# Kernel optimization log

Measured on AMD Instinct MI355X. Metric: run time of the kernel, lower is better.

Reference implementation:

```python
import jax, jax.numpy as jnp
import numpy as np

EPS = 1e-5

def _conv(x, w, b, stride, pad):
    y = jax.lax.conv_general_dilated(
        x, w, window_strides=(stride, stride),
        padding=[(pad, pad), (pad, pad)],
        dimension_numbers=('NCHW', 'OIHW', 'NCHW'))
    return y + b.reshape(1, -1, 1, 1)

def _bn(x, gamma, beta):
    # training-mode batch norm: per-channel batch statistics over (N, H, W)
    mean = jnp.mean(x, axis=(0, 2, 3), keepdims=True)
    var = jnp.var(x, axis=(0, 2, 3), keepdims=True)
    xn = (x - mean) * jax.lax.rsqrt(var + EPS)
    return gamma.reshape(1, -1, 1, 1) * xn + beta.reshape(1, -1, 1, 1)

def setup_inputs() -> dict:
    key = jax.random.key(0)
    ks = jax.random.split(key, 8)
    N, Cin, H, W = 64, 1024, 14, 14
    P = 256                      # planes (bottleneck width)
    Cout = P * 4                 # expansion = 4 -> 1024
    def kaiming(k, shape):
        fan_in = shape[1] * shape[2] * shape[3]
        return jax.random.normal(k, shape, jnp.float32) * np.float32(np.sqrt(2.0 / fan_in))
    return {
        'x':  jax.random.normal(ks[0], (N, Cin, H, W), jnp.float32),
        'w1': kaiming(ks[1], (P, Cin, 1, 1)),  'b1': jnp.zeros((P,), jnp.float32),
        'g1': jnp.ones((P,), jnp.float32),     'be1': jnp.zeros((P,), jnp.float32),
        'w2': kaiming(ks[2], (P, P, 3, 3)),    'b2': jnp.zeros((P,), jnp.float32),
        'g2': jnp.ones((P,), jnp.float32),     'be2': jnp.zeros((P,), jnp.float32),
        'w3': kaiming(ks[3], (Cout, P, 1, 1)), 'b3': jnp.zeros((Cout,), jnp.float32),
        'g3': jnp.ones((Cout,), jnp.float32),  'be3': jnp.zeros((Cout,), jnp.float32),
        'residual_scale': jnp.zeros((1,), jnp.float32),
    }

def reference(x, w1, b1, g1, be1, w2, b2, g2, be2, w3, b3, g3, be3, residual_scale):
    out = jax.nn.relu(_bn(_conv(x, w1, b1, 1, 0), g1, be1))   # 1x1 reduce
    out = jax.nn.relu(_bn(_conv(out, w2, b2, 1, 1), g2, be2)) # 3x3
    out = _bn(_conv(out, w3, b3, 1, 0), g3, be3)              # 1x1 expand
    out = jax.nn.softplus(residual_scale)[0] * out            # scaled residual branch
    out = x + out                                             # identity shortcut (stride=1, Cin==Cout)
    return jax.nn.relu(out)
```

## Files before the change

kernel.cpp:

```cpp
#include <hip/hip_runtime.h>
#include <hip/hip_bf16.h>
#include <cstdint>

#define NB   64
#define CIN  1024
#define HWSP 196
#define MTOT 12544
#define PL   256
#define COUT 1024

using f32x4 = __attribute__((ext_vector_type(4))) float;
using s16x8 = __attribute__((ext_vector_type(8))) short;

static __device__ __forceinline__ short f2bf(float f) {
  union { __hip_bfloat16 h; short s; } u;
  u.h = __float2bfloat16(f);
  return u.s;
}
static __device__ __forceinline__ float bf2f(short s) {
  union { float f; unsigned u; } x;
  x.u = ((unsigned)(unsigned short)s) << 16;
  return x.f;
}

static __device__ __forceinline__ void gload16(const void* g, void* l) {
  __builtin_amdgcn_global_load_lds((const __attribute__((address_space(1))) void*)g,
                                   (__attribute__((address_space(3))) void*)l, 16, 0, 0);
}

__global__ __launch_bounds__(256) void k_prep(const float* __restrict__ x,
                                              const float* __restrict__ w1,
                                              const float* __restrict__ w2,
                                              const float* __restrict__ w3,
                                              short* __restrict__ xb,
                                              short* __restrict__ w1b,
                                              short* __restrict__ w2b,
                                              short* __restrict__ w3b,
                                              float* __restrict__ statszero) {
  const int bid = blockIdx.x;
  if (bid < 2048) {
    __shared__ float tile[32][197];
    const int n = bid >> 5;
    const int c0 = (bid & 31) * 32;
    for (int idx = threadIdx.x; idx < 32 * 196; idx += 256) {
      int cl = idx / 196, hw = idx % 196;
      tile[cl][hw] = x[((size_t)(n * CIN + c0 + cl)) * HWSP + hw];
    }
    __syncthreads();
    for (int idx = threadIdx.x; idx < 196 * 32; idx += 256) {
      int hw = idx >> 5, cl = idx & 31;
      xb[((size_t)(n * HWSP + hw)) * CIN + c0 + cl] = f2bf(tile[cl][hw]);
    }
  } else if (bid < 6400) {
    int i = (bid - 2048) * 256 + threadIdx.x;
    if (i < 262144) w1b[i] = f2bf(w1[i]);
    int j = i - 262144;
    if (j >= 0 && j < 589824) {
      int co = j / 2304, rem = j % 2304;
      int d = rem >> 8, ci = rem & 255;
      w2b[j] = f2bf(w2[((size_t)(co * 256 + ci)) * 9 + d]);
    }
    int k = i - 851968;
    if (k >= 0 && k < 262144) w3b[k] = f2bf(w3[k]);
  } else {
    for (int k = threadIdx.x; k < 3136; k += 256) statszero[k] = 0.f;
  }
}

static __device__ __forceinline__ int swz(int row, int k16) {
  return row * 128 + (((unsigned)(k16 ^ (row & 7))) << 4);
}

template <int MODE, int K, int BM, int BN>
__global__ __launch_bounds__(256) void gemm_kernel(const short* __restrict__ A,
                                                   const short* __restrict__ Bw,
                                                   const float* __restrict__ bias,
                                                   short* __restrict__ Yb,
                                                   float* __restrict__ st,
                                                   int Nc,
                                                   const short* __restrict__ zerobuf) {
  constexpr int MI = BM / 32;
  constexpr int NJ = BN / 32;
  constexpr int ABYTES = BM * 128;
  __shared__ __align__(16) char lds[2][BM * 128 + BN * 128];

  const int m0 = blockIdx.x * BM;
  const int n0 = blockIdx.y * BN;
  const int t = threadIdx.x;
  const int lane = t & 63, wid = t >> 6;
  const int wm = wid >> 1, wn = wid & 1;
  const int g = lane >> 4, r = lane & 15;
  constexpr int NKT = K >> 6;

  const short* aSrc[MI];
  int aN[MI], aH[MI], aW[MI], aCi[MI];
#pragma unroll
  for (int q = 0; q < MI; ++q) {
    int chunk = t + q * 256;
    int row = chunk >> 3;
    int k16s = (chunk & 7) ^ (row & 7);
    if (MODE == 0) {
      aSrc[q] = A + (size_t)(m0 + row) * K + k16s * 8;
    } else {
      int m = m0 + row;
      int n_ = m / 196;
      int hw = m - n_ * 196;
      aN[q] = n_;
      aH[q] = hw / 14;
      aW[q] = hw - aH[q] * 14;
      aCi[q] = k16s * 8;
    }
  }
  const short* bSrc[NJ];
#pragma unroll
  for (int q = 0; q < NJ; ++q) {
    int chunk = t + q * 256;
    int row = chunk >> 3;
    int k16s = (chunk & 7) ^ (row & 7);
    bSrc[q] = Bw + (size_t)(n0 + row) * K + k16s * 8;
  }

  auto stage = [&](int buf, int kt) {
    const int k0 = kt << 6;
    char* dA = &lds[buf][0];
    char* dB = &lds[buf][ABYTES];
#pragma unroll
    for (int q = 0; q < MI; ++q) {
      const short* s;
      if (MODE == 0) {
        s = aSrc[q] + k0;
      } else {
        int d = kt >> 2;
        int dh = d / 3, dw = d - dh * 3;
        int hh = aH[q] + dh - 1, ww = aW[q] + dw - 1;
        s = ((unsigned)hh < 14u && (unsigned)ww < 14u)
                ? A + ((size_t)(aN[q] * 196 + hh * 14 + ww)) * 256 + (k0 & 255) + aCi[q]
                : zerobuf;
      }
      gload16(s, dA + (t + q * 256) * 16);
    }
#pragma unroll
    for (int q = 0; q < NJ; ++q)
      gload16(bSrc[q] + k0, dB + (t + q * 256) * 16);
  };

  f32x4 acc[MI][NJ] = {};
  auto compute = [&](int buf) {
    char* baseA = &lds[buf][0];
    char* baseB = &lds[buf][ABYTES];
#pragma unroll
    for (int ks = 0; ks < 2; ++ks) {
      s16x8 af[MI], bfr[NJ];
#pragma unroll
      for (int i = 0; i < MI; ++i)
        af[i] = *(const s16x8*)(baseA + swz(wm * (BM / 2) + i * 16 + r, ks * 4 + g));
#pragma unroll
      for (int j = 0; j < NJ; ++j)
        bfr[j] = *(const s16x8*)(baseB + swz(wn * (BN / 2) + j * 16 + r, ks * 4 + g));
#pragma unroll
      for (int i = 0; i < MI; ++i)
#pragma unroll
        for (int j = 0; j < NJ; ++j)
          acc[i][j] = __builtin_amdgcn_mfma_f32_16x16x32_bf16(af[i], bfr[j], acc[i][j], 0, 0, 0);
    }
  };

  stage(0, 0);
  __syncthreads();
  int cur = 0;
#pragma unroll 1
  for (int kt = 0; kt < NKT - 1; ++kt) {
    stage(cur ^ 1, kt + 1);
    compute(cur);
    __syncthreads();
    cur ^= 1;
  }
  compute(cur);

#pragma unroll
  for (int j = 0; j < NJ; ++j) {
    int col = n0 + wn * (BN / 2) + j * 16 + r;
    float bv = bias[col];
    float ps = 0.f, pq = 0.f;
#pragma unroll
    for (int i = 0; i < MI; ++i) {
      int row_base = m0 + wm * (BM / 2) + i * 16 + g * 4;
#pragma unroll
      for (int rr = 0; rr < 4; ++rr) {
        float v = acc[i][j][rr] + bv;
        ps += v;
        pq += v * v;
        Yb[(size_t)(row_base + rr) * Nc + col] = f2bf(v);
      }
    }
    ps += __shfl_xor(ps, 16);
    ps += __shfl_xor(ps, 32);
    pq += __shfl_xor(pq, 16);
    pq += __shfl_xor(pq, 32);
    if (lane < 16) {
      atomicAdd(&st[col], ps);
      atomicAdd(&st[Nc + col], pq);
    }
  }
}

__global__ __launch_bounds__(256) void k_apply(short* __restrict__ Yb,
                                               const float* __restrict__ st,
                                               const float* __restrict__ gamma,
                                               const float* __restrict__ beta) {
  __shared__ float lsc[256], lsh[256];
  const int t = threadIdx.x;
  {
    const float inv = 1.0f / 12544.0f;
    float mean = st[t] * inv;
    float var = st[256 + t] * inv - mean * mean;
    float s = gamma[t] * rsqrtf(var + 1e-5f);
    lsc[t] = s;
    lsh[t] = beta[t] - mean * s;
  }
  __syncthreads();
  size_t i8 = ((size_t)blockIdx.x * 256 + t) * 8;
  s16x8 v = *(const s16x8*)(Yb + i8);
  int c0 = (int)(i8 & 255);
#pragma unroll
  for (int e = 0; e < 8; ++e) {
    float f = bf2f(v[e]);
    v[e] = f2bf(fmaxf(lsc[c0 + e] * f + lsh[c0 + e], 0.f));
  }
  *(s16x8*)(Yb + i8) = v;
}

__global__ __launch_bounds__(256) void k_final(const float* __restrict__ x,
                                               const short* __restrict__ y3b,
                                               const float* __restrict__ st,
                                               const float* __restrict__ gamma,
                                               const float* __restrict__ beta,
                                               const float* __restrict__ rs,
                                               float* __restrict__ out) {
  __shared__ short ytile[64][198];
  __shared__ float lsc[64], lsh[64];
  const int n = blockIdx.x;
  const int co0 = blockIdx.y * 64;
  const int t = threadIdx.x;
  if (t < 64) {
    const float inv = 1.0f / 12544.0f;
    int c = co0 + t;
    float mean = st[c] * inv;
    float var = st[1024 + c] * inv - mean * mean;
    float s = gamma[c] * rsqrtf(var + 1e-5f);
    lsc[t] = s;
    lsh[t] = beta[c] - mean * s;
  }
#pragma unroll
  for (int iter = 0; iter < 49; ++iter) {
    int idx = iter * 256 + t;
    int hw = idx >> 6, c = idx & 63;
    ytile[c][hw] = y3b[((size_t)(n * 196 + hw)) * 1024 + co0 + c];
  }
  __syncthreads();
  float z = rs[0];
  float s = fmaxf(z, 0.f) + log1pf(expf(-fabsf(z)));
#pragma unroll
  for (int iter = 0; iter < 49; ++iter) {
    int idx = iter * 256 + t;
    int co = idx / 196, hw = idx - co * 196;
    size_t xi = ((size_t)(n * 1024 + co0 + co)) * 196 + hw;
    float v = bf2f(ytile[co][hw]);
    float o = x[xi] + s * (lsc[co] * v + lsh[co]);
    out[xi] = fmaxf(o, 0.f);
  }
}

extern "C" void kernel_launch(void* const* d_in, const int* in_sizes, int n_in,
                              void* d_out, int out_size, void* d_ws, size_t ws_size,
                              hipStream_t stream) {
  const float* x   = (const float*)d_in[0];
  const float* w1  = (const float*)d_in[1];
  const float* b1  = (const float*)d_in[2];
  const float* g1  = (const float*)d_in[3];
  const float* be1 = (const float*)d_in[4];
  const float* w2  = (const float*)d_in[5];
  const float* b2  = (const float*)d_in[6];
  const float* g2  = (const float*)d_in[7];
  const float* be2 = (const float*)d_in[8];
  const float* w3  = (const float*)d_in[9];
  const float* b3  = (const float*)d_in[10];
  const float* g3  = (const float*)d_in[11];
  const float* be3 = (const float*)d_in[12];
  const float* rs  = (const float*)d_in[13];
  float* out = (float*)d_out;
  char* ws = (char*)d_ws;

  size_t off = 0;
  auto alloc = [&](size_t bytes) {
    size_t o = off;
    off += (bytes + 255) & ~(size_t)255;
    return o;
  };
  short* xb  = (short*)(ws + alloc((size_t)MTOT * CIN * 2));
  short* w1b = (short*)(ws + alloc((size_t)262144 * 2));
  short* w2b = (short*)(ws + alloc((size_t)589824 * 2));
  short* w3b = (short*)(ws + alloc((size_t)262144 * 2));
  short* y1b = (short*)(ws + alloc((size_t)MTOT * PL * 2));
  short* y2b = (short*)(ws + alloc((size_t)MTOT * PL * 2));
  short* y3b = (short*)(ws + alloc((size_t)MTOT * COUT * 2));
  float* stats = (float*)(ws + alloc(12288 + 256));
  float* stat1 = stats, *stat2 = stats + 512, *stat3 = stats + 1024;
  short* zerobuf = (short*)(stats + 3072);

  k_prep<<<6401, 256, 0, stream>>>(x, w1, w2, w3, xb, w1b, w2b, w3b, stats);

  gemm_kernel<0, 1024, 128, 64><<<dim3(98, 4), 256, 0, stream>>>(xb, w1b, b1, y1b, stat1, 256, zerobuf);
  k_apply<<<1568, 256, 0, stream>>>(y1b, stat1, g1, be1);

  gemm_kernel<1, 2304, 64, 128><<<dim3(196, 2), 256, 0, stream>>>(y1b, w2b, b2, y2b, stat2, 256, zerobuf);
  k_apply<<<1568, 256, 0, stream>>>(y2b, stat2, g2, be2);

  gemm_kernel<0, 256, 128, 128><<<dim3(98, 8), 256, 0, stream>>>(y2b, w3b, b3, y3b, stat3, 1024, zerobuf);

  k_final<<<dim3(64, 16), 256, 0, stream>>>(x, y3b, stat3, g3, be3, rs, out);
}
```

Measured before the change: 129.5 us.

## Fuse batch-norm apply and ReLU into first two GEMMs via grid-wide barrier

Removes the two separate k_apply launches. Each GEMM block now accumulates bias-free channel statistics, waits on an atomic counter until all 392 blocks are done, then applies the normalization and ReLU straight from its accumulators before writing bf16 output. This saves a full read and write of the intermediate tensors and two launches. It relies on all 392 blocks being resident at once to avoid deadlock, and the spin wait adds a grid-wide stall at the end of each GEMM.

```diff
diff --git a/kernel.cpp b/kernel.cpp
--- a/kernel.cpp
+++ b/kernel.cpp
@@ -63,7 +63,7 @@
     int k = i - 851968;
     if (k >= 0 && k < 262144) w3b[k] = f2bf(w3[k]);
   } else {
-    for (int k = threadIdx.x; k < 3136; k += 256) statszero[k] = 0.f;
+    for (int k = threadIdx.x; k < 3200; k += 256) statszero[k] = 0.f;
   }
 }
 
@@ -71,13 +71,16 @@
   return row * 128 + (((unsigned)(k16 ^ (row & 7))) << 4);
 }
 
-template <int MODE, int K, int BM, int BN>
+template <int MODE, int K, int BM, int BN, int FUSE>
 __global__ __launch_bounds__(256) void gemm_kernel(const short* __restrict__ A,
                                                    const short* __restrict__ Bw,
                                                    const float* __restrict__ bias,
+                                                   const float* __restrict__ gamma,
+                                                   const float* __restrict__ beta,
                                                    short* __restrict__ Yb,
                                                    float* __restrict__ st,
-                                                   int Nc,
+                                                   unsigned* __restrict__ cnt,
+                                                   int nblk, int Nc,
                                                    const short* __restrict__ zerobuf) {
   constexpr int MI = BM / 32;
   constexpr int NJ = BN / 32;
@@ -177,57 +180,85 @@
   }
   compute(cur);
 
-#pragma unroll
-  for (int j = 0; j < NJ; ++j) {
-    int col = n0 + wn * (BN / 2) + j * 16 + r;
-    float bv = bias[col];
-    float ps = 0.f, pq = 0.f;
-#pragma unroll
-    for (int i = 0; i < MI; ++i) {
-      int row_base = m0 + wm * (BM / 2) + i * 16 + g * 4;
-#pragma unroll
-      for (int rr = 0; rr < 4; ++rr) {
-        float v = acc[i][j][rr] + bv;
-        ps += v;
-        pq += v * v;
-        Yb[(size_t)(row_base + rr) * Nc + col] = f2bf(v);
-      }
-    }
-    ps += __shfl_xor(ps, 16);
-    ps += __shfl_xor(ps, 32);
-    pq += __shfl_xor(pq, 16);
-    pq += __shfl_xor(pq, 32);
-    if (lane < 16) {
-      atomicAdd(&st[col], ps);
-      atomicAdd(&st[Nc + col], pq);
-    }
-  }
-}
-
-__global__ __launch_bounds__(256) void k_apply(short* __restrict__ Yb,
-                                               const float* __restrict__ st,
-                                               const float* __restrict__ gamma,
-                                               const float* __restrict__ beta) {
-  __shared__ float lsc[256], lsh[256];
-  const int t = threadIdx.x;
-  {
+  if (FUSE == 0) {
+#pragma unroll
+    for (int j = 0; j < NJ; ++j) {
+      int col = n0 + wn * (BN / 2) + j * 16 + r;
+      float bv = bias[col];
+      float ps = 0.f, pq = 0.f;
+#pragma unroll
+      for (int i = 0; i < MI; ++i) {
+        int row_base = m0 + wm * (BM / 2) + i * 16 + g * 4;
+#pragma unroll
+        for (int rr = 0; rr < 4; ++rr) {
+          float v = acc[i][j][rr] + bv;
+          ps += v;
+          pq += v * v;
+          Yb[(size_t)(row_base + rr) * Nc + col] = f2bf(v);
+        }
+      }
+      ps += __shfl_xor(ps, 16);
+      ps += __shfl_xor(ps, 32);
+      pq += __shfl_xor(pq, 16);
+      pq += __shfl_xor(pq, 32);
+      if (lane < 16) {
+        atomicAdd(&st[col], ps);
+        atomicAdd(&st[Nc + col], pq);
+      }
+    }
+  } else {
+#pragma unroll
+    for (int j = 0; j < NJ; ++j) {
+      int col = n0 + wn * (BN / 2) + j * 16 + r;
+      float ps = 0.f, pq = 0.f;
+#pragma unroll
+      for (int i = 0; i < MI; ++i)
+#pragma unroll
+        for (int rr = 0; rr < 4; ++rr) {
+          float v = acc[i][j][rr];
+          ps += v;
+          pq += v * v;
+        }
+      ps += __shfl_xor(ps, 16);
+      ps += __shfl_xor(ps, 32);
+      pq += __shfl_xor(pq, 16);
+      pq += __shfl_xor(pq, 32);
+      if (lane < 16) {
+        atomicAdd(&st[col], ps);
+        atomicAdd(&st[Nc + col], pq);
+      }
+    }
+    __syncthreads();
+    if (t == 0) {
+      __threadfence();
+      __hip_atomic_fetch_add(cnt, 1u, __ATOMIC_ACQ_REL, __HIP_MEMORY_SCOPE_AGENT);
+      while (__hip_atomic_load(cnt, __ATOMIC_ACQUIRE, __HIP_MEMORY_SCOPE_AGENT) <
+             (unsigned)nblk) {
+        __builtin_amdgcn_s_sleep(8);
+      }
+    }
+    __syncthreads();
     const float inv = 1.0f / 12544.0f;
-    float mean = st[t] * inv;
-    float var = st[256 + t] * inv - mean * mean;
-    float s = gamma[t] * rsqrtf(var + 1e-5f);
-    lsc[t] = s;
-    lsh[t] = beta[t] - mean * s;
-  }
-  __syncthreads();
-  size_t i8 = ((size_t)blockIdx.x * 256 + t) * 8;
-  s16x8 v = *(const s16x8*)(Yb + i8);
-  int c0 = (int)(i8 & 255);
-#pragma unroll
-  for (int e = 0; e < 8; ++e) {
-    float f = bf2f(v[e]);
-    v[e] = f2bf(fmaxf(lsc[c0 + e] * f + lsh[c0 + e], 0.f));
-  }
-  *(s16x8*)(Yb + i8) = v;
+#pragma unroll
+    for (int j = 0; j < NJ; ++j) {
+      int col = n0 + wn * (BN / 2) + j * 16 + r;
+      float s0 = __hip_atomic_load(&st[col], __ATOMIC_RELAXED, __HIP_MEMORY_SCOPE_AGENT);
+      float q0 = __hip_atomic_load(&st[Nc + col], __ATOMIC_RELAXED, __HIP_MEMORY_SCOPE_AGENT);
+      float mean_raw = s0 * inv;
+      float var = q0 * inv - mean_raw * mean_raw;
+      float sc = gamma[col] * rsqrtf(var + 1e-5f);
+      float sh = beta[col] - (mean_raw + bias[col]) * sc;
+#pragma unroll
+      for (int i = 0; i < MI; ++i) {
+        int row_base = m0 + wm * (BM / 2) + i * 16 + g * 4;
+#pragma unroll
+        for (int rr = 0; rr < 4; ++rr) {
+          float v = fmaxf(sc * acc[i][j][rr] + sh, 0.f);
+          Yb[(size_t)(row_base + rr) * Nc + col] = f2bf(v);
+        }
+      }
+    }
+  }
 }
 
 __global__ __launch_bounds__(256) void k_final(const float* __restrict__ x,
@@ -304,19 +335,22 @@
   short* y1b = (short*)(ws + alloc((size_t)MTOT * PL * 2));
   short* y2b = (short*)(ws + alloc((size_t)MTOT * PL * 2));
   short* y3b = (short*)(ws + alloc((size_t)MTOT * COUT * 2));
-  float* stats = (float*)(ws + alloc(12288 + 256));
+  float* stats = (float*)(ws + alloc(3200 * 4));
   float* stat1 = stats, *stat2 = stats + 512, *stat3 = stats + 1024;
-  short* zerobuf = (short*)(stats + 3072);
+  unsigned* cnt1 = (unsigned*)(stats + 3072);
+  unsigned* cnt2 = (unsigned*)(stats + 3073);
+  short* zerobuf = (short*)(stats + 3136);
 
   k_prep<<<6401, 256, 0, stream>>>(x, w1, w2, w3, xb, w1b, w2b, w3b, stats);
 
-  gemm_kernel<0, 1024, 128, 64><<<dim3(98, 4), 256, 0, stream>>>(xb, w1b, b1, y1b, stat1, 256, zerobuf);
-  k_apply<<<1568, 256, 0, stream>>>(y1b, stat1, g1, be1);
-
-  gemm_kernel<1, 2304, 64, 128><<<dim3(196, 2), 256, 0, stream>>>(y1b, w2b, b2, y2b, stat2, 256, zerobuf);
-  k_apply<<<1568, 256, 0, stream>>>(y2b, stat2, g2, be2);
-
-  gemm_kernel<0, 256, 128, 128><<<dim3(98, 8), 256, 0, stream>>>(y2b, w3b, b3, y3b, stat3, 1024, zerobuf);
+  gemm_kernel<0, 1024, 128, 64, 1><<<dim3(98, 4), 256, 0, stream>>>(
+      xb, w1b, b1, g1, be1, y1b, stat1, cnt1, 392, 256, zerobuf);
+
+  gemm_kernel<1, 2304, 64, 128, 1><<<dim3(196, 2), 256, 0, stream>>>(
+      y1b, w2b, b2, g2, be2, y2b, stat2, cnt2, 392, 256, zerobuf);
+
+  gemm_kernel<0, 256, 128, 128, 0><<<dim3(98, 8), 256, 0, stream>>>(
+      y2b, w3b, b3, g3, be3, y3b, stat3, nullptr, 0, 1024, zerobuf);
 
   k_final<<<dim3(64, 16), 256, 0, stream>>>(x, y3b, stat3, g3, be3, rs, out);
 }
```

New measurement: 184.7 us. 1.43x slower.
